# Kernel optimization log

Measured on AMD Instinct MI355X. Metric: run time of the kernel, lower is better.

## Reference

```python
import jax, jax.numpy as jnp
import numpy as np

N_NODES = 50000
N_EDGES = 800000
IN_C, HID_C, OUT_C = 128, 128, 64
BN_EPS = 1e-5


def _normalized_adj(edge_index, N):
    # Mirrors remove_self_loops + add_self_loops + symmetric GCN normalization.
    src, dst = edge_index[0], edge_index[1]
    mask = (src != dst).astype(jnp.float32)  # drop original self loops
    # degree of dst over (masked edges + added self loops)
    deg = jax.ops.segment_sum(mask, dst, num_segments=N) + 1.0
    dinv = jnp.where(deg > 0, deg ** -0.5, 0.0)
    w = mask * dinv[src] * dinv[dst]          # weights for original edges
    w_self = dinv * dinv                      # weights for added self loops
    return src, dst, w, w_self


def _spmm(src, dst, w, w_self, x):
    # torch.sparse.mm(adj, x): out[i] = sum_{e: src[e]=i} w[e] * x[dst[e]] + w_self[i]*x[i]
    agg = jax.ops.segment_sum(w[:, None] * x[dst], src, num_segments=x.shape[0])
    return agg + w_self[:, None] * x


def setup_inputs() -> dict:
    key = jax.random.key(0)
    ks = jax.random.split(key, 4)
    x = jax.random.normal(ks[0], (N_NODES, IN_C), dtype=jnp.float32)
    edge_index = jax.random.randint(ks[1], (2, N_EDGES), 0, N_NODES, dtype=jnp.int64)
    # glorot init for GCN linear weights
    s1 = np.sqrt(6.0 / (IN_C + HID_C)).astype(np.float32)
    s2 = np.sqrt(6.0 / (HID_C + OUT_C)).astype(np.float32)
    W1 = jax.random.uniform(ks[2], (IN_C, HID_C), jnp.float32, -s1, s1)
    W2 = jax.random.uniform(ks[3], (HID_C, OUT_C), jnp.float32, -s2, s2)
    return {
        "x": x,
        "edge_index": edge_index,
        "W1": W1,
        "b1": jnp.zeros((HID_C,), jnp.float32),
        "gamma": jnp.ones((HID_C,), jnp.float32),
        "beta": jnp.zeros((HID_C,), jnp.float32),
        "W2": W2,
        "b2": jnp.zeros((OUT_C,), jnp.float32),
    }


def reference(x, edge_index, W1, b1, gamma, beta, W2, b2):
    N = x.shape[0]
    src, dst, w, w_self = _normalized_adj(edge_index, N)
    # layer 1: linear -> SpMM -> BN (batch stats) -> ReLU (dropout: eval)
    h = x @ W1 + b1
    h = _spmm(src, dst, w, w_self, h)
    mean = h.mean(axis=0)
    var = jnp.mean((h - mean) ** 2, axis=0)
    h = (h - mean) * jax.lax.rsqrt(var + BN_EPS) * gamma + beta
    h = jax.nn.relu(h)
    # layer 2: linear -> SpMM
    h = h @ W2 + b2
    h = _spmm(src, dst, w, w_self, h)
    return h
```

## Files before the change

kernel.cpp:

```cpp
#include <hip/hip_runtime.h>

#define N_NODES 50000
#define N_EDGES 800000
#define BN_EPS 1e-5f
#define NPAD 50176
#define SCAN_BLOCKS 98

#define S_SLICES 64
#define R_RANGES 4
#define BINS 16384
#define NP4 (R_RANGES * BINS)
#define ES (N_EDGES / S_SLICES)

#define XS_STRIDE 68

#define NB_FILL (S_SLICES * R_RANGES)

typedef unsigned int uint;
typedef unsigned short ushort;
typedef unsigned char uchar;
typedef float floatx4 __attribute__((ext_vector_type(4)));
typedef short bf16x8 __attribute__((ext_vector_type(8)));

__device__ __forceinline__ float bfl(uint u) { return __uint_as_float(u << 16); }
__device__ __forceinline__ float bfh(uint u) { return __uint_as_float(u & 0xffff0000u); }
__device__ __forceinline__ uint pack_bf2(float a, float b) {
    uint ua = __float_as_uint(a), ub = __float_as_uint(b);
    ua += 0x7fffu + ((ua >> 16) & 1u);
    ub += 0x7fffu + ((ub >> 16) & 1u);
    return (ua >> 16) | (ub & 0xffff0000u);
}
__device__ __forceinline__ ushort bf1(float x) {
    uint u = __float_as_uint(x);
    u += 0x7fffu + ((u >> 16) & 1u);
    return (ushort)(u >> 16);
}
__device__ __forceinline__ void acc8(float* a, uint4 h, float w) {
    a[0] += w * bfl(h.x); a[1] += w * bfh(h.x);
    a[2] += w * bfl(h.y); a[3] += w * bfh(h.y);
    a[4] += w * bfl(h.z); a[5] += w * bfh(h.z);
    a[6] += w * bfl(h.w); a[7] += w * bfh(h.w);
}

__global__ __launch_bounds__(1024) void count_hist_kernel(const int* __restrict__ src,
                                                          const int* __restrict__ dst,
                                                          const float* __restrict__ W1,
                                                          const float* __restrict__ W2,
                                                          uint* __restrict__ W1t,
                                                          uint* __restrict__ W2t,
                                                          uchar* __restrict__ part_cnt,
                                                          uchar* __restrict__ part_deg) {
    if (blockIdx.x == NB_FILL) {
        for (int t = threadIdx.x; t < 12288; t += 1024) {
            if (t < 8192) {
                int n = t >> 6, kk = t & 63;
                W1t[t] = pack_bf2(W1[(2 * kk) * 128 + n], W1[(2 * kk + 1) * 128 + n]);
            } else {
                int u = t - 8192;
                int n = u >> 6, kk = u & 63;
                W2t[u] = pack_bf2(W2[(2 * kk) * 64 + n], W2[(2 * kk + 1) * 64 + n]);
            }
        }
        return;
    }
    __shared__ uint cnt_lds[BINS / 4];
    __shared__ uint deg_lds[BINS / 4];
    const int s = blockIdx.x / R_RANGES;
    const int r = blockIdx.x % R_RANGES;
    const int base = r * BINS;
    for (int j = threadIdx.x; j < BINS / 4; j += 1024) { cnt_lds[j] = 0u; deg_lds[j] = 0u; }
    __syncthreads();
    const int4* s4 = (const int4*)(src + s * ES);
    const int4* d4 = (const int4*)(dst + s * ES);
    for (int g = threadIdx.x; g < ES / 4; g += 1024) {
        int4 sv = s4[g];
        int4 dv = d4[g];
#pragma unroll
        for (int k = 0; k < 4; ++k) {
            int ss = (&sv.x)[k], dd = (&dv.x)[k];
            if (ss != dd) {
                int a = ss - base;
                if ((unsigned)a < (unsigned)BINS)
                    atomicAdd(&cnt_lds[a >> 2], 1u << ((a & 3) * 8));
                int b = dd - base;
                if ((unsigned)b < (unsigned)BINS)
                    atomicAdd(&deg_lds[b >> 2], 1u << ((b & 3) * 8));
            }
        }
    }
    __syncthreads();
    uint* pc = (uint*)&part_cnt[s * NP4 + base];
    uint* pd = (uint*)&part_deg[s * NP4 + base];
    for (int j = threadIdx.x; j < BINS / 4; j += 1024) { pc[j] = cnt_lds[j]; pd[j] = deg_lds[j]; }
}

__global__ __launch_bounds__(256) void reduce_scan_kernel(const uchar* __restrict__ part_deg,
                                                          const uchar* __restrict__ part_cnt,
                                                          float* __restrict__ dinv,
                                                          int* __restrict__ rowcnt,
                                                          int* __restrict__ rowptr,
                                                          int* __restrict__ psum,
                                                          float* __restrict__ stats) {
    const int t = threadIdx.x;
    if (blockIdx.x == 0) stats[t] = 0.f;
    const int i = blockIdx.x * 512 + 2 * t;
    uint dg0 = 0, dg1 = 0, rc0 = 0, rc1 = 0;
#pragma unroll 8
    for (int s = 0; s < S_SLICES; ++s) {
        uint vd = *(const ushort*)&part_deg[s * NP4 + i];
        uint vc = *(const ushort*)&part_cnt[s * NP4 + i];
        dg0 += vd & 0xffu; dg1 += vd >> 8;
        rc0 += vc & 0xffu; rc1 += vc >> 8;
    }
    *(int2*)&rowcnt[i] = make_int2((int)rc0, (int)rc1);
    if (i < N_NODES) dinv[i] = rsqrtf((float)dg0 + 1.0f);
    if (i + 1 < N_NODES) dinv[i + 1] = rsqrtf((float)dg1 + 1.0f);

    __shared__ int bs[256];
    const int pair = (int)(rc0 + rc1);
    bs[t] = pair;
    __syncthreads();
#pragma unroll
    for (int off = 1; off < 256; off <<= 1) {
        int x = (t >= off) ? bs[t - off] : 0;
        __syncthreads();
        bs[t] += x;
        __syncthreads();
    }
    const int excl = bs[t] - pair;
    *(int2*)&rowptr[i] = make_int2(excl + (int)rc0, excl + pair);
    if (t == 255) psum[blockIdx.x] = bs[255];
}

__global__ __launch_bounds__(256) void cursor_init_kernel(const int* __restrict__ rowcnt,
                                                          int* __restrict__ rowptr,
                                                          const int* __restrict__ psum,
                                                          const uchar* __restrict__ part_cnt,
                                                          ushort* __restrict__ pre) {
    __shared__ int pbuf[SCAN_BLOCKS];
    __shared__ int lps;
    const int t = threadIdx.x;
    if (t < SCAN_BLOCKS) pbuf[t] = psum[t];
    __syncthreads();
    if (t == 0) {
        int acc = 0;
        for (int j = 0; j < (int)blockIdx.x; ++j) acc += pbuf[j];
        lps = acc;
    }
    __syncthreads();
    const int ps = lps;
    const int i = blockIdx.x * 512 + 2 * t;
    int b0 = rowptr[i] - rowcnt[i] + ps;
    int b1 = rowptr[i + 1] - rowcnt[i + 1] + ps;
    *(int2*)&rowptr[i] = make_int2(b0, b1);
    uint p0 = 0, p1 = 0;
#pragma unroll 8
    for (int s = 0; s < S_SLICES; ++s) {
        *(ushort2*)&pre[s * NP4 + i] = make_ushort2((ushort)p0, (ushort)p1);
        uint vc = *(const ushort*)&part_cnt[s * NP4 + i];
        p0 += vc & 0xffu;
        p1 += vc >> 8;
    }
}

__global__ __launch_bounds__(1024) void fill_lds_kernel(const int* __restrict__ src,
                                                        const int* __restrict__ dst,
                                                        const float* __restrict__ dinv,
                                                        const int* __restrict__ rowptr,
                                                        const ushort* __restrict__ pre,
                                                        int2* __restrict__ epair) {
    __shared__ int curs[BINS];
    const int t = threadIdx.x;
    const int s = blockIdx.x / R_RANGES;
    const int r = blockIdx.x % R_RANGES;
    const int base = r * BINS;
    const ushort* pr = &pre[s * NP4 + base];
    for (int j = t; j < BINS; j += 1024) {
        int node = base + j;
        int rp = (node < NPAD) ? rowptr[node] : 0;
        curs[j] = rp + (int)pr[j];
    }
    __syncthreads();
    const int4* s4 = (const int4*)(src + s * ES);
    const int4* d4 = (const int4*)(dst + s * ES);
    for (int g = t; g < ES / 4; g += 1024) {
        int4 sv = s4[g];
        int4 dv = d4[g];
#pragma unroll
        for (int k = 0; k < 4; ++k) {
            int ss = (&sv.x)[k], dd = (&dv.x)[k];
            int a = ss - base;
            if (ss != dd && (unsigned)a < (unsigned)BINS) {
                int pos = atomicAdd(&curs[a], 1);
                epair[pos] = make_int2(dd, __float_as_int(dinv[ss] * dinv[dd]));
            }
        }
    }
}

__global__ __launch_bounds__(256) void gemm1_mfma_kernel(const float* __restrict__ X,
                                                         const uint* __restrict__ W1t,
                                                         const float* __restrict__ bias,
                                                         ushort* __restrict__ Hbf) {
    __shared__ uint lds[(64 + 128) * XS_STRIDE];
    uint* Xs = lds;
    uint* Ws = lds + 64 * XS_STRIDE;
    const int t = threadIdx.x;
    const int rowBase = blockIdx.x * 64;

    {
        int r = t >> 2, q = t & 3;
        int arow = rowBase + r;
        uint* xd = &Xs[r * XS_STRIDE + q * 16];
        if (arow < N_NODES) {
            const float4* xp = (const float4*)&X[arow * 128 + q * 32];
#pragma unroll
            for (int i = 0; i < 8; ++i) {
                float4 v = xp[i];
                xd[2 * i]     = pack_bf2(v.x, v.y);
                xd[2 * i + 1] = pack_bf2(v.z, v.w);
            }
        } else {
#pragma unroll
            for (int i = 0; i < 16; ++i) xd[i] = 0u;
        }
    }
    {
        int n = t >> 1, half = t & 1;
        const uint4* wp = (const uint4*)&W1t[n * 64 + half * 32];
        uint* wd = &Ws[n * XS_STRIDE + half * 32];
#pragma unroll
        for (int i = 0; i < 8; ++i) *(uint4*)&wd[i * 4] = wp[i];
    }
    __syncthreads();

    const int wv = t >> 6, lane = t & 63;
    const int lr = lane & 15;
    const int ko = (lane >> 4) * 4;
    const int m0 = wv * 16;
    floatx4 acc[8];
#pragma unroll
    for (int j = 0; j < 8; ++j) acc[j] = (floatx4){0.f, 0.f, 0.f, 0.f};

#pragma unroll
    for (int ks = 0; ks < 4; ++ks) {
        const int kb = ks * 16 + ko;
        bf16x8 a = *(bf16x8*)&Xs[(m0 + lr) * XS_STRIDE + kb];
#pragma unroll
        for (int j = 0; j < 8; ++j) {
            bf16x8 b = *(bf16x8*)&Ws[(j * 16 + lr) * XS_STRIDE + kb];
            acc[j] = __builtin_amdgcn_mfma_f32_16x16x32_bf16(a, b, acc[j], 0, 0, 0);
        }
    }
    const int rbase = rowBase + m0 + (lane >> 4) * 4;
#pragma unroll
    for (int j = 0; j < 8; ++j) {
        const int col = j * 16 + lr;
        const float bb = bias[col];
#pragma unroll
        for (int r = 0; r < 4; ++r) {
            int row = rbase + r;
            if (row < N_NODES) Hbf[row * 128 + col] = bf1(acc[j][r] + bb);
        }
    }
}

__global__ __launch_bounds__(256) void gemm2_mfma_kernel(const uint* __restrict__ Hin,
                                                         const uint* __restrict__ W2t,
                                                         const float* __restrict__ bias,
                                                         const float* __restrict__ sum,
                                                         const float* __restrict__ sumsq,
                                                         const float* __restrict__ gamma,
                                                         const float* __restrict__ beta,
                                                         ushort* __restrict__ Hbf) {
    __shared__ uint lds[(64 + 64) * XS_STRIDE];
    __shared__ float sc_sh[128], sh_sh[128];
    uint* Xs = lds;
    uint* Ws = lds + 64 * XS_STRIDE;
    const int t = threadIdx.x;
    const int rowBase = blockIdx.x * 64;

    if (t < 128) {
        float mean = sum[t] * (1.0f / N_NODES);
        float var = sumsq[t] * (1.0f / N_NODES) - mean * mean;
        float sc = gamma[t] * rsqrtf(var + BN_EPS);
        sc_sh[t] = sc;
        sh_sh[t] = beta[t] - mean * sc;
    }
    if (t >= 128) {
        int u = t - 128;
        int n = u >> 1, half = u & 1;
        const uint4* wp = (const uint4*)&W2t[n * 64 + half * 32];
        uint* wd = &Ws[n * XS_STRIDE + half * 32];
#pragma unroll
        for (int i = 0; i < 8; ++i) *(uint4*)&wd[i * 4] = wp[i];
    }
    __syncthreads();

    {
        int r = t >> 2, q = t & 3;
        int arow = rowBase + r;
        uint* xd = &Xs[r * XS_STRIDE + q * 16];
        if (arow < N_NODES) {
            const uint* hp = &Hin[arow * 64 + q * 16];
#pragma unroll
            for (int i = 0; i < 16; ++i) {
                uint u = hp[i];
                int m = q * 16 + i;
                float a0 = fmaxf(0.f, bfl(u) * sc_sh[2 * m] + sh_sh[2 * m]);
                float a1 = fmaxf(0.f, bfh(u) * sc_sh[2 * m + 1] + sh_sh[2 * m + 1]);
                xd[i] = pack_bf2(a0, a1);
            }
        } else {
#pragma unroll
            for (int i = 0; i < 16; ++i) xd[i] = 0u;
        }
    }
    __syncthreads();

    const int wv = t >> 6, lane = t & 63;
    const int lr = lane & 15;
    const int ko = (lane >> 4) * 4;
    const int m0 = wv * 16;
    floatx4 acc[4];
#pragma unroll
    for (int j = 0; j < 4; ++j) acc[j] = (floatx4){0.f, 0.f, 0.f, 0.f};

#pragma unroll
    for (int ks = 0; ks < 4; ++ks) {
        const int kb = ks * 16 + ko;
        bf16x8 a = *(bf16x8*)&Xs[(m0 + lr) * XS_STRIDE + kb];
#pragma unroll
        for (int j = 0; j < 4; ++j) {
            bf16x8 b = *(bf16x8*)&Ws[(j * 16 + lr) * XS_STRIDE + kb];
            acc[j] = __builtin_amdgcn_mfma_f32_16x16x32_bf16(a, b, acc[j], 0, 0, 0);
        }
    }
    const int rbase = rowBase + m0 + (lane >> 4) * 4;
#pragma unroll
    for (int j = 0; j < 4; ++j) {
        const int col = j * 16 + lr;
        const float bb = bias[col];
#pragma unroll
        for (int r = 0; r < 4; ++r) {
            int row = rbase + r;
            if (row < N_NODES) Hbf[row * 64 + col] = bf1(acc[j][r] + bb);
        }
    }
}

template <int C, bool OUT_BF16>
__global__ __launch_bounds__(256) void spmm_bf16_kernel(const int* __restrict__ rowptr,
                                                        const int2* __restrict__ epair,
                                                        const float* __restrict__ dinv,
                                                        const uint* __restrict__ H,
                                                        void* __restrict__ outv) {
    constexpr int LPR = C / 8;
    constexpr int TPR = LPR * 2;
    constexpr int RPB = 256 / TPR;
    constexpr int US  = C / 2;
    const int t = threadIdx.x;
    const int lane = t % LPR;
    const int g = (t / LPR) & 1;
    const int row = blockIdx.x * RPB + t / TPR;
    const int cu = lane * 4;

    float acc[8];
#pragma unroll
    for (int j = 0; j < 8; ++j) acc[j] = 0.f;
    if (g == 0) {
        const float di = dinv[row];
        uint4 hv = *(const uint4*)&H[row * US + cu];
        acc8(acc, hv, di * di);
    }
    const int e0 = rowptr[row], e1 = rowptr[row + 1];
    int lo = e0, hi = e1;
    if (lo & 1) {
        if (g == 0 && lo < hi) {
            int2 p = epair[lo];
            uint4 h = *(const uint4*)&H[p.x * US + cu];
            acc8(acc, h, __int_as_float(p.y));
        }
        ++lo;
    }
    if (lo < hi && (hi & 1)) {
        --hi;
        if (g == 1) {
            int2 p = epair[hi];
            uint4 h = *(const uint4*)&H[p.x * US + cu];
            acc8(acc, h, __int_as_float(p.y));
        }
    }
    const int4* ep4 = (const int4*)epair;
    int p = (lo >> 1) + g;
    const int pe = hi >> 1;
    for (; p + 6 < pe; p += 8) {
        int4 qa = ep4[p + 0];
        int4 qb = ep4[p + 2];
        int4 qc = ep4[p + 4];
        int4 qd = ep4[p + 6];
        uint4 h0 = *(const uint4*)&H[qa.x * US + cu];
        uint4 h1 = *(const uint4*)&H[qa.z * US + cu];
        uint4 h2 = *(const uint4*)&H[qb.x * US + cu];
        uint4 h3 = *(const uint4*)&H[qb.z * US + cu];
        uint4 h4 = *(const uint4*)&H[qc.x * US + cu];
        uint4 h5 = *(const uint4*)&H[qc.z * US + cu];
        uint4 h6 = *(const uint4*)&H[qd.x * US + cu];
        uint4 h7 = *(const uint4*)&H[qd.z * US + cu];
        acc8(acc, h0, __int_as_float(qa.y));
        acc8(acc, h1, __int_as_float(qa.w));
        acc8(acc, h2, __int_as_float(qb.y));
        acc8(acc, h3, __int_as_float(qb.w));
        acc8(acc, h4, __int_as_float(qc.y));
        acc8(acc, h5, __int_as_float(qc.w));
        acc8(acc, h6, __int_as_float(qd.y));
        acc8(acc, h7, __int_as_float(qd.w));
    }
    for (; p < pe; p += 2) {
        int4 q = ep4[p];
        uint4 h0 = *(const uint4*)&H[q.x * US + cu];
        uint4 h1 = *(const uint4*)&H[q.z * US + cu];
        acc8(acc, h0, __int_as_float(q.y));
        acc8(acc, h1, __int_as_float(q.w));
    }
#pragma unroll
    for (int j = 0; j < 8; ++j) acc[j] += __shfl_xor(acc[j], LPR, 64);
    if (g != 0) return;
    if (OUT_BF16) {
        uint4 o;
        o.x = pack_bf2(acc[0], acc[1]);
        o.y = pack_bf2(acc[2], acc[3]);
        o.z = pack_bf2(acc[4], acc[5]);
        o.w = pack_bf2(acc[6], acc[7]);
        *(uint4*)&((uint*)outv)[row * US + cu] = o;
    } else {
        float* out = (float*)outv;
        *(float4*)&out[row * C + lane * 8]     = make_float4(acc[0], acc[1], acc[2], acc[3]);
        *(float4*)&out[row * C + lane * 8 + 4] = make_float4(acc[4], acc[5], acc[6], acc[7]);
    }
}

__global__ __launch_bounds__(256) void bn_stats_kernel(const uint* __restrict__ H,
                                                       float* __restrict__ sum,
                                                       float* __restrict__ sumsq) {
    int uc = threadIdx.x & 63;
    int quarter = threadIdx.x >> 6;
    const int stride = gridDim.x * 4;
    float s0 = 0.f, q0 = 0.f, s1 = 0.f, q1 = 0.f;
    for (int r = blockIdx.x * 4 + quarter; r < N_NODES; r += stride) {
        uint u = H[r * 64 + uc];
        float a = bfl(u), b = bfh(u);
        s0 += a; q0 += a * a;
        s1 += b; q1 += b * b;
    }
    __shared__ float red[4][256];
    red[0][threadIdx.x] = s0; red[1][threadIdx.x] = q0;
    red[2][threadIdx.x] = s1; red[3][threadIdx.x] = q1;
    __syncthreads();
    if (quarter == 0) {
        float ts0 = 0.f, tq0 = 0.f, ts1 = 0.f, tq1 = 0.f;
#pragma unroll
        for (int k = 0; k < 4; ++k) {
            ts0 += red[0][k * 64 + uc]; tq0 += red[1][k * 64 + uc];
            ts1 += red[2][k * 64 + uc]; tq1 += red[3][k * 64 + uc];
        }
        atomicAdd(&sum[2 * uc], ts0);
        atomicAdd(&sum[2 * uc + 1], ts1);
        atomicAdd(&sumsq[2 * uc], tq0);
        atomicAdd(&sumsq[2 * uc + 1], tq1);
    }
}

extern "C" void kernel_launch(void* const* d_in, const int* in_sizes, int n_in,
                              void* d_out, int out_size, void* d_ws, size_t ws_size,
                              hipStream_t stream) {
    const float* x     = (const float*)d_in[0];
    const int*   ei    = (const int*)d_in[1];
    const float* W1    = (const float*)d_in[2];
    const float* b1    = (const float*)d_in[3];
    const float* gamma = (const float*)d_in[4];
    const float* beta  = (const float*)d_in[5];
    const float* W2    = (const float*)d_in[6];
    const float* b2    = (const float*)d_in[7];
    float* out = (float*)d_out;
    const int* src = ei;
    const int* dst = ei + N_EDGES;

    float* ws     = (float*)d_ws;
    float* dinv   = ws;
    float* stats  = ws + NPAD;
    int*   psum   = (int*)(ws + NPAD + 512);
    int*   rowcnt = psum + 128;
    int*   rowptr = rowcnt + NPAD;
    float* big    = (float*)(rowptr + NPAD);
    int2*   epair    = (int2*)big;
    uchar*  part_cnt = (uchar*)(big + 1600000);
    uchar*  part_deg = (uchar*)(big + 3700000);
    ushort* pre      = (ushort*)(big + 5800000);
    ushort* h1bf     = (ushort*)(big + 1600000);
    uint*   h1agg    = (uint*)(big + 4800000);
    ushort* h2bf     = h1bf;
    uint*   W1t      = (uint*)(big + 10000000);
    uint*   W2t      = W1t + 8192;
    float* sum    = stats;
    float* sumsq  = stats + 128;

    count_hist_kernel<<<NB_FILL + 1, 1024, 0, stream>>>(src, dst, W1, W2, W1t, W2t,
                                                        part_cnt, part_deg);
    reduce_scan_kernel<<<SCAN_BLOCKS, 256, 0, stream>>>(part_deg, part_cnt, dinv, rowcnt,
                                                        rowptr, psum, stats);
    cursor_init_kernel<<<SCAN_BLOCKS, 256, 0, stream>>>(rowcnt, rowptr, psum, part_cnt, pre);
    fill_lds_kernel<<<NB_FILL, 1024, 0, stream>>>(src, dst, dinv, rowptr, pre, epair);

    gemm1_mfma_kernel<<<(N_NODES + 63) / 64, 256, 0, stream>>>(x, W1t, b1, h1bf);

    spmm_bf16_kernel<128, true><<<N_NODES / 8, 256, 0, stream>>>(
        rowptr, epair, dinv, (const uint*)h1bf, (void*)h1agg);

    bn_stats_kernel<<<250, 256, 0, stream>>>(h1agg, sum, sumsq);

    gemm2_mfma_kernel<<<(N_NODES + 63) / 64, 256, 0, stream>>>(h1agg, W2t, b2, sum, sumsq,
                                                               gamma, beta, h2bf);

    spmm_bf16_kernel<64, false><<<N_NODES / 16, 256, 0, stream>>>(
        rowptr, epair, dinv, (const uint*)h2bf, (void*)out);
}
```

Measured before the change: 240.4 us.

## Store only edge destinations and factor dinv out of SpMM weights

Fill no longer computes and stores per-edge weights; it writes only the destination index, which halves the CSR edge array. SpMM looks up dinv[d] for each neighbor and multiplies by the row's dinv once at the end, relying on the factorization w = dinv[src]*dinv[dst]. Each row is now split across four thread groups instead of two, using an extra shuffle reduction and twice the blocks. The trade is an extra dependent gather of dinv per edge in exchange for less index traffic and more parallelism per row.

```diff
diff --git a/kernel.cpp b/kernel.cpp
--- a/kernel.cpp
+++ b/kernel.cpp
@@ -165,10 +165,9 @@
 
 __global__ __launch_bounds__(1024) void fill_lds_kernel(const int* __restrict__ src,
                                                         const int* __restrict__ dst,
-                                                        const float* __restrict__ dinv,
                                                         const int* __restrict__ rowptr,
                                                         const ushort* __restrict__ pre,
-                                                        int2* __restrict__ epair) {
+                                                        int* __restrict__ edst) {
     __shared__ int curs[BINS];
     const int t = threadIdx.x;
     const int s = blockIdx.x / R_RANGES;
@@ -192,7 +191,7 @@
             int a = ss - base;
             if (ss != dd && (unsigned)a < (unsigned)BINS) {
                 int pos = atomicAdd(&curs[a], 1);
-                epair[pos] = make_int2(dd, __float_as_int(dinv[ss] * dinv[dd]));
+                edst[pos] = dd;
             }
         }
     }
@@ -351,92 +350,66 @@
 
 template <int C, bool OUT_BF16>
 __global__ __launch_bounds__(256) void spmm_bf16_kernel(const int* __restrict__ rowptr,
-                                                        const int2* __restrict__ epair,
+                                                        const int* __restrict__ edst,
                                                         const float* __restrict__ dinv,
                                                         const uint* __restrict__ H,
                                                         void* __restrict__ outv) {
     constexpr int LPR = C / 8;
-    constexpr int TPR = LPR * 2;
+    constexpr int TPR = LPR * 4;
     constexpr int RPB = 256 / TPR;
     constexpr int US  = C / 2;
     const int t = threadIdx.x;
     const int lane = t % LPR;
-    const int g = (t / LPR) & 1;
+    const int g = (t / LPR) & 3;
     const int row = blockIdx.x * RPB + t / TPR;
     const int cu = lane * 4;
+    const float di = dinv[row];
 
     float acc[8];
 #pragma unroll
     for (int j = 0; j < 8; ++j) acc[j] = 0.f;
     if (g == 0) {
-        const float di = dinv[row];
         uint4 hv = *(const uint4*)&H[row * US + cu];
-        acc8(acc, hv, di * di);
+        acc8(acc, hv, di);
     }
     const int e0 = rowptr[row], e1 = rowptr[row + 1];
-    int lo = e0, hi = e1;
-    if (lo & 1) {
-        if (g == 0 && lo < hi) {
-            int2 p = epair[lo];
-            uint4 h = *(const uint4*)&H[p.x * US + cu];
-            acc8(acc, h, __int_as_float(p.y));
-        }
-        ++lo;
-    }
-    if (lo < hi && (hi & 1)) {
-        --hi;
-        if (g == 1) {
-            int2 p = epair[hi];
-            uint4 h = *(const uint4*)&H[p.x * US + cu];
-            acc8(acc, h, __int_as_float(p.y));
-        }
-    }
-    const int4* ep4 = (const int4*)epair;
-    int p = (lo >> 1) + g;
-    const int pe = hi >> 1;
-    for (; p + 6 < pe; p += 8) {
-        int4 qa = ep4[p + 0];
-        int4 qb = ep4[p + 2];
-        int4 qc = ep4[p + 4];
-        int4 qd = ep4[p + 6];
-        uint4 h0 = *(const uint4*)&H[qa.x * US + cu];
-        uint4 h1 = *(const uint4*)&H[qa.z * US + cu];
-        uint4 h2 = *(const uint4*)&H[qb.x * US + cu];
-        uint4 h3 = *(const uint4*)&H[qb.z * US + cu];
-        uint4 h4 = *(const uint4*)&H[qc.x * US + cu];
-        uint4 h5 = *(const uint4*)&H[qc.z * US + cu];
-        uint4 h6 = *(const uint4*)&H[qd.x * US + cu];
-        uint4 h7 = *(const uint4*)&H[qd.z * US + cu];
-        acc8(acc, h0, __int_as_float(qa.y));
-        acc8(acc, h1, __int_as_float(qa.w));
-        acc8(acc, h2, __int_as_float(qb.y));
-        acc8(acc, h3, __int_as_float(qb.w));
-        acc8(acc, h4, __int_as_float(qc.y));
-        acc8(acc, h5, __int_as_float(qc.w));
-        acc8(acc, h6, __int_as_float(qd.y));
-        acc8(acc, h7, __int_as_float(qd.w));
-    }
-    for (; p < pe; p += 2) {
-        int4 q = ep4[p];
-        uint4 h0 = *(const uint4*)&H[q.x * US + cu];
-        uint4 h1 = *(const uint4*)&H[q.z * US + cu];
-        acc8(acc, h0, __int_as_float(q.y));
-        acc8(acc, h1, __int_as_float(q.w));
+    int e = e0 + g;
+    for (; e + 12 < e1; e += 16) {
+        int d0 = edst[e], d1 = edst[e + 4], d2 = edst[e + 8], d3 = edst[e + 12];
+        float w0 = dinv[d0], w1 = dinv[d1], w2 = dinv[d2], w3 = dinv[d3];
+        uint4 h0 = *(const uint4*)&H[d0 * US + cu];
+        uint4 h1 = *(const uint4*)&H[d1 * US + cu];
+        uint4 h2 = *(const uint4*)&H[d2 * US + cu];
+        uint4 h3 = *(const uint4*)&H[d3 * US + cu];
+        acc8(acc, h0, w0);
+        acc8(acc, h1, w1);
+        acc8(acc, h2, w2);
+        acc8(acc, h3, w3);
+    }
+    for (; e < e1; e += 4) {
+        int d = edst[e];
+        float w = dinv[d];
+        uint4 h = *(const uint4*)&H[d * US + cu];
+        acc8(acc, h, w);
     }
 #pragma unroll
     for (int j = 0; j < 8; ++j) acc[j] += __shfl_xor(acc[j], LPR, 64);
+#pragma unroll
+    for (int j = 0; j < 8; ++j) acc[j] += __shfl_xor(acc[j], 2 * LPR, 64);
     if (g != 0) return;
     if (OUT_BF16) {
         uint4 o;
-        o.x = pack_bf2(acc[0], acc[1]);
-        o.y = pack_bf2(acc[2], acc[3]);
-        o.z = pack_bf2(acc[4], acc[5]);
-        o.w = pack_bf2(acc[6], acc[7]);
+        o.x = pack_bf2(acc[0] * di, acc[1] * di);
+        o.y = pack_bf2(acc[2] * di, acc[3] * di);
+        o.z = pack_bf2(acc[4] * di, acc[5] * di);
+        o.w = pack_bf2(acc[6] * di, acc[7] * di);
         *(uint4*)&((uint*)outv)[row * US + cu] = o;
     } else {
         float* out = (float*)outv;
-        *(float4*)&out[row * C + lane * 8]     = make_float4(acc[0], acc[1], acc[2], acc[3]);
-        *(float4*)&out[row * C + lane * 8 + 4] = make_float4(acc[4], acc[5], acc[6], acc[7]);
+        *(float4*)&out[row * C + lane * 8] =
+            make_float4(acc[0] * di, acc[1] * di, acc[2] * di, acc[3] * di);
+        *(float4*)&out[row * C + lane * 8 + 4] =
+            make_float4(acc[4] * di, acc[5] * di, acc[6] * di, acc[7] * di);
     }
 }
 
@@ -493,7 +466,7 @@
     int*   rowcnt = psum + 128;
     int*   rowptr = rowcnt + NPAD;
     float* big    = (float*)(rowptr + NPAD);
-    int2*   epair    = (int2*)big;
+    int*    edst     = (int*)big;
     uchar*  part_cnt = (uchar*)(big + 1600000);
     uchar*  part_deg = (uchar*)(big + 3700000);
     ushort* pre      = (ushort*)(big + 5800000);
@@ -510,18 +483,18 @@
     reduce_scan_kernel<<<SCAN_BLOCKS, 256, 0, stream>>>(part_deg, part_cnt, dinv, rowcnt,
                                                         rowptr, psum, stats);
     cursor_init_kernel<<<SCAN_BLOCKS, 256, 0, stream>>>(rowcnt, rowptr, psum, part_cnt, pre);
-    fill_lds_kernel<<<NB_FILL, 1024, 0, stream>>>(src, dst, dinv, rowptr, pre, epair);
+    fill_lds_kernel<<<NB_FILL, 1024, 0, stream>>>(src, dst, rowptr, pre, edst);
 
     gemm1_mfma_kernel<<<(N_NODES + 63) / 64, 256, 0, stream>>>(x, W1t, b1, h1bf);
 
-    spmm_bf16_kernel<128, true><<<N_NODES / 8, 256, 0, stream>>>(
-        rowptr, epair, dinv, (const uint*)h1bf, (void*)h1agg);
+    spmm_bf16_kernel<128, true><<<N_NODES / 4, 256, 0, stream>>>(
+        rowptr, edst, dinv, (const uint*)h1bf, (void*)h1agg);
 
     bn_stats_kernel<<<250, 256, 0, stream>>>(h1agg, sum, sumsq);
 
     gemm2_mfma_kernel<<<(N_NODES + 63) / 64, 256, 0, stream>>>(h1agg, W2t, b2, sum, sumsq,
                                                                gamma, beta, h2bf);
 
-    spmm_bf16_kernel<64, false><<<N_NODES / 16, 256, 0, stream>>>(
-        rowptr, epair, dinv, (const uint*)h2bf, (void*)out);
-}
+    spmm_bf16_kernel<64, false><<<N_NODES / 8, 256, 0, stream>>>(
+        rowptr, edst, dinv, (const uint*)h2bf, (void*)out);
+}
```

Result: faster. 228.3 us, median of 2 (-5.0%).
